# Performance work log

Measured on AMD Instinct MI355X. Metric: run time of the kernel, lower is better.

The kernel has to match this reference:

```python
import jax, jax.numpy as jnp
import numpy as np

B, N, D, H, F = 16, 512, 768, 8, 96  # D == H*F, dims preserved across layers
NEG_INF = -1e20


def setup_inputs() -> dict:
    key = jax.random.key(0)
    ks = jax.random.split(key, 16)
    embeddings = jax.random.normal(ks[0], (B, N, D), dtype=jnp.float32)
    # 0/1 float adjacency with self-loops so no row is fully masked
    adj = (jax.random.uniform(ks[1], (B, N, N)) < 0.3).astype(jnp.float32)
    adj = jnp.maximum(adj, jnp.eye(N, dtype=jnp.float32)[None])
    convo_len = jnp.full((B,), N, dtype=jnp.int32)

    def layer_params(k0, k1, k2, k3, k4, in_dim, out_dim):
        sW = (2.0 / (in_dim + out_dim)) ** 0.5  # ~xavier
        sa = (2.0 / (out_dim + 1)) ** 0.5
        sH = (2.0 / (in_dim + in_dim)) ** 0.5
        return dict(
            W=jax.random.normal(k0, (H, in_dim, out_dim)) * sW,
            b=jnp.zeros((out_dim,), jnp.float32),
            a_src=jax.random.normal(k1, (H, out_dim, 1)) * sa,
            a_dst=jax.random.normal(k2, (H, out_dim, 1)) * sa,
            Hw=jax.random.normal(k3, (in_dim, in_dim)) * sH,
            Hb=jnp.zeros((in_dim,), jnp.float32),
        )

    p0 = layer_params(ks[2], ks[3], ks[4], ks[5], ks[6], D, F)
    p1 = layer_params(ks[7], ks[8], ks[9], ks[10], ks[11], D, F)
    return {
        "embeddings": embeddings, "adj": adj, "convo_len": convo_len,
        "W0": p0["W"], "b0": p0["b"], "a_src0": p0["a_src"], "a_dst0": p0["a_dst"], "Hw0": p0["Hw"], "Hb0": p0["Hb"],
        "W1": p1["W"], "b1": p1["b"], "a_src1": p1["a_src"], "a_dst1": p1["a_dst"], "Hw1": p1["Hw"], "Hb1": p1["Hb"],
    }


def gat_layer(x, adj, W, b, a_src, a_dst, Hw, Hb):
    b_, n_, _ = x.shape
    h_, _, f_ = W.shape
    h = jnp.einsum('bni,hio->bhno', x, W)            # [B,H,N,F]
    t = jnp.tanh(h)
    s = jnp.einsum('bhno,ho->bhn', t, a_src[..., 0])  # attn_src
    d = jnp.einsum('bhno,ho->bhn', t, a_dst[..., 0])  # attn_dst
    attn = jax.nn.leaky_relu(s[:, :, :, None] + d[:, :, None, :], 0.2)  # [B,H,N,N]
    attn = jnp.where(adj[:, None, :, :] > 0, attn, NEG_INF)
    attn = jax.nn.softmax(attn, axis=-1)
    out = jnp.einsum('bhij,bhjo->bhio', attn, h) + b  # [B,H,N,F]
    # faithful to torch: transpose(0,1).contiguous().view(batch, N, -1)
    out = jnp.transpose(out, (1, 0, 2, 3)).reshape(b_, n_, h_ * f_)
    out = jax.nn.elu(out)
    gate = jax.nn.sigmoid(x @ Hw.T + Hb)
    return gate * out + (1.0 - gate) * x


def reference(embeddings, adj, convo_len,
              W0, b0, a_src0, a_dst0, Hw0, Hb0,
              W1, b1, a_src1, a_dst1, Hw1, Hb1):
    x = gat_layer(embeddings, adj, W0, b0, a_src0, a_dst0, Hw0, Hb0)
    x = gat_layer(x, adj, W1, b1, a_src1, a_dst1, Hw1, Hb1)
    return x
```

## Files before the change

kernel.cpp:

```cpp
#include <hip/hip_runtime.h>
#include <cstdint>
#include <cstddef>

typedef __attribute__((ext_vector_type(4))) float f32x4;
typedef __attribute__((ext_vector_type(8))) __bf16 bf16x8;
typedef __attribute__((ext_vector_type(8))) unsigned short u16x8;
typedef __attribute__((ext_vector_type(4))) unsigned short u16x4;

__device__ __forceinline__ unsigned short f2bf(float f){
  unsigned int u = __float_as_uint(f);
  u += 0x7fffu + ((u >> 16) & 1u);
  return (unsigned short)(u >> 16);
}
__device__ __forceinline__ float bf2f(unsigned short u){
  return __uint_as_float(((unsigned int)u) << 16);
}
__device__ __forceinline__ float fast_tanh(float x){
  const float e = __expf(2.f * x);
  return 1.f - 2.f / (e + 1.f);
}

__device__ __forceinline__ void gload_lds16(const void* g, void* l){
  __builtin_amdgcn_global_load_lds((const __attribute__((address_space(1))) void*)g,
                                   (__attribute__((address_space(3))) void*)l, 16, 0, 0);
}

__device__ __forceinline__ f32x4 mfma16(bf16x8 a, bf16x8 b, f32x4 c){
  return __builtin_amdgcn_mfma_f32_16x16x32_bf16(a, b, c, 0, 0, 0);
}

__global__ __launch_bounds__(256) void prep_kernel(const float* __restrict__ in,
                                                   unsigned short* __restrict__ out,
                                                   const float* __restrict__ adj,
                                                   unsigned int* __restrict__ mask,
                                                   const float* __restrict__ W0,
                                                   const float* __restrict__ Hw0,
                                                   unsigned short* __restrict__ Bt0,
                                                   const float* __restrict__ W1,
                                                   const float* __restrict__ Hw1,
                                                   unsigned short* __restrict__ Bt1){
  const int bid = blockIdx.x;
  if (bid < 6144){
    int i = bid * 256 + threadIdx.x;
    f32x4 v = ((const f32x4*)in)[i];
    union { unsigned short u[4]; unsigned long long ll; } o;
    #pragma unroll
    for (int e = 0; e < 4; ++e) o.u[e] = f2bf(v[e]);
    ((unsigned long long*)out)[i] = o.ll;
  } else if (bid < 6656){
    int idx = (bid - 6144) * 256 + threadIdx.x;
    const float* a = adj + (size_t)idx * 32;
    unsigned int m = 0;
    #pragma unroll
    for (int e = 0; e < 8; ++e){
      f32x4 v = *(const f32x4*)(a + e * 4);
      m |= (v[0] > 0.f ? 1u : 0u) << (e * 4);
      m |= (v[1] > 0.f ? 1u : 0u) << (e * 4 + 1);
      m |= (v[2] > 0.f ? 1u : 0u) << (e * 4 + 2);
      m |= (v[3] > 0.f ? 1u : 0u) << (e * 4 + 3);
    }
    mask[idx] = m;
  } else {
    const int rel = bid - 6656;
    const int layer = rel >= 1536;
    const int n = layer ? rel - 1536 : rel;
    const float* W  = layer ? W1  : W0;
    const float* Hw = layer ? Hw1 : Hw0;
    unsigned short* Bt = layer ? Bt1 : Bt0;
    const int k4 = threadIdx.x;
    if (k4 < 192){
      float v[4];
      if (n < 768){
        int head = n / 96, f = n % 96;
        const float* base = W + (size_t)head * 768 * 96 + f;
        #pragma unroll
        for (int e = 0; e < 4; ++e) v[e] = base[(size_t)(k4 * 4 + e) * 96];
      } else {
        f32x4 t = *(const f32x4*)(Hw + (size_t)(n - 768) * 768 + k4 * 4);
        #pragma unroll
        for (int e = 0; e < 4; ++e) v[e] = t[e];
      }
      union { unsigned short u[4]; unsigned long long ll; } o;
      #pragma unroll
      for (int e = 0; e < 4; ++e) o.u[e] = f2bf(v[e]);
      ((unsigned long long*)(Bt + (size_t)n * 768))[k4] = o.ll;
    }
  }
}

__global__ __launch_bounds__(256, 3)
void gemm_kernel(const unsigned short* __restrict__ A,
                 const unsigned short* __restrict__ Bt,
                 const float* __restrict__ Hb,
                 unsigned short* __restrict__ hT,
                 unsigned short* __restrict__ glogit){
  __shared__ __align__(16) char lds[49152];
  const int tid  = threadIdx.x;
  const int wid  = tid >> 6;
  const int lane = tid & 63;
  const int orig = blockIdx.x;
  const int wgid = (orig & 7) * 192 + (orig >> 3);
  const int mtile = wgid / 24, ntile = wgid % 24;
  const int m0 = mtile * 128, n0 = ntile * 64;
  const int wm = (wid >> 1) * 64, wn = (wid & 1) * 32;
  const int g = lane >> 4, r16 = lane & 15;

  auto stage = [&](int kt, char* base){
    #pragma unroll
    for (int c = 0; c < 4; ++c){
      const int ch = c * 256 + tid;
      const int row = ch >> 3, sp = ch & 7;
      const int cj = sp ^ (row & 7);
      gload_lds16(A + (size_t)(m0 + row) * 768 + kt * 64 + cj * 8, base + ch * 16);
    }
    #pragma unroll
    for (int c = 0; c < 2; ++c){
      const int ch = c * 256 + tid;
      const int row = ch >> 3, sp = ch & 7;
      const int cj = sp ^ (row & 7);
      gload_lds16(Bt + (size_t)(n0 + row) * 768 + kt * 64 + cj * 8, base + 16384 + ch * 16);
    }
  };

  f32x4 acc[4][2];
  #pragma unroll
  for (int i = 0; i < 4; ++i)
    #pragma unroll
    for (int j = 0; j < 2; ++j) acc[i][j] = (f32x4){0.f, 0.f, 0.f, 0.f};

  stage(0, lds);
  __syncthreads();

  for (int kt = 0; kt < 12; ++kt){
    const int cur = kt & 1;
    if (kt < 11) stage(kt + 1, lds + (cur ^ 1) * 24576);
    const char* base = lds + cur * 24576;
    bf16x8 af[4][2], bfr[2][2];
    #pragma unroll
    for (int t = 0; t < 4; ++t){
      const int rowA = wm + t * 16 + r16;
      #pragma unroll
      for (int kk = 0; kk < 2; ++kk){
        const int ckk = (kk << 2) | g;
        af[t][kk] = *(const bf16x8*)(base + rowA * 128 + ((ckk ^ (rowA & 7)) << 4));
      }
    }
    #pragma unroll
    for (int nt = 0; nt < 2; ++nt){
      const int rowB = wn + nt * 16 + r16;
      #pragma unroll
      for (int kk = 0; kk < 2; ++kk){
        const int ckk = (kk << 2) | g;
        bfr[nt][kk] = *(const bf16x8*)(base + 16384 + rowB * 128 + ((ckk ^ (rowB & 7)) << 4));
      }
    }
    #pragma unroll
    for (int mt = 0; mt < 4; ++mt)
      #pragma unroll
      for (int nt = 0; nt < 2; ++nt){
        acc[mt][nt] = mfma16(af[mt][0], bfr[nt][0], acc[mt][nt]);
        acc[mt][nt] = mfma16(af[mt][1], bfr[nt][1], acc[mt][nt]);
      }
    __syncthreads();
  }

  if (n0 < 768){
    #pragma unroll
    for (int mt = 0; mt < 4; ++mt){
      #pragma unroll
      for (int nt = 0; nt < 2; ++nt){
        const int n_local = wn + nt * 16 + r16;
        const int m_base  = wm + mt * 16 + g * 4;
        union { unsigned short u[4]; unsigned long long ll; } pk;
        #pragma unroll
        for (int r = 0; r < 4; ++r) pk.u[r] = f2bf(acc[mt][nt][r]);
        const int byte = m_base * 2;
        const int chunk = byte >> 4, o = byte & 15;
        const int pbyte = n_local * 256 + ((chunk ^ (n_local & 15)) << 4) + o;
        *(unsigned long long*)(lds + pbyte) = pk.ll;
      }
    }
    __syncthreads();
    const int b_ = m0 >> 9, nodebase = m0 & 511;
    #pragma unroll
    for (int it = 0; it < 4; ++it){
      const int ci = it * 256 + tid;
      const int row = ci >> 4, l = ci & 15;
      const int pbyte = row * 256 + (((l ^ (row & 15))) << 4);
      f32x4 v = *(const f32x4*)(lds + pbyte);
      const int n = n0 + row, head = n / 96, f = n % 96;
      *(f32x4*)(hT + (((size_t)(b_ * 8 + head)) * 96 + f) * 512 + nodebase + l * 8) = v;
    }
  } else {
    #pragma unroll
    for (int mt = 0; mt < 4; ++mt){
      #pragma unroll
      for (int nt = 0; nt < 2; ++nt){
        const int n_local = wn + nt * 16 + r16;
        const float hbv = Hb[n0 - 768 + n_local];
        const int c = n_local >> 3;
        #pragma unroll
        for (int r = 0; r < 4; ++r){
          const int m_local = wm + mt * 16 + g * 4 + r;
          const int pbyte = m_local * 128 + ((c ^ (m_local & 7)) << 4) + (n_local & 7) * 2;
          *(unsigned short*)(lds + pbyte) = f2bf(acc[mt][nt][r] + hbv);
        }
      }
    }
    __syncthreads();
    const int colbase = n0 - 768;
    #pragma unroll
    for (int it = 0; it < 4; ++it){
      const int ci = it * 256 + tid;
      const int row = ci >> 3, l = ci & 7;
      const int pbyte = row * 128 + ((l ^ (row & 7)) << 4);
      f32x4 v = *(const f32x4*)(lds + pbyte);
      *(f32x4*)(glogit + (size_t)(m0 + row) * 768 + colbase + l * 8) = v;
    }
  }
}

__global__ __launch_bounds__(256)
void sd_kernel(const unsigned short* __restrict__ hT, const float* __restrict__ asrc,
               const float* __restrict__ adst, float* __restrict__ s, float* __restrict__ d){
  const int bh = blockIdx.x;
  const int tid = threadIdx.x;
  const int head = bh & 7;
  __shared__ float as_lds[96], ad_lds[96];
  if (tid < 96) as_lds[tid] = asrc[head * 96 + tid];
  else if (tid >= 128 && tid < 224) ad_lds[tid - 128] = adst[head * 96 + tid - 128];
  __syncthreads();

  const unsigned short* hTb = hT + (size_t)bh * 96 * 512 + tid * 2;
  float s0 = 0.f, s1 = 0.f, d0 = 0.f, d1 = 0.f;
  #pragma unroll 8
  for (int f = 0; f < 96; ++f){
    const unsigned int u = *(const unsigned int*)(hTb + (size_t)f * 512);
    const float t0 = fast_tanh(bf2f((unsigned short)(u & 0xffffu)));
    const float t1 = fast_tanh(bf2f((unsigned short)(u >> 16)));
    const float a = as_lds[f], dd = ad_lds[f];
    s0 += t0 * a;  s1 += t1 * a;
    d0 += t0 * dd; d1 += t1 * dd;
  }
  const int o = (bh << 9) + tid * 2;
  *(float2*)(s + o) = make_float2(s0, s1);
  *(float2*)(d + o) = make_float2(d0, d1);
}

__global__ __launch_bounds__(256)
void attn_kernel(const float* __restrict__ s, const float* __restrict__ d,
                 const unsigned int* __restrict__ mask,
                 const unsigned short* __restrict__ hT,
                 const float* __restrict__ bias,
                 const unsigned short* __restrict__ glogit,
                 const float* __restrict__ xin,
                 float* __restrict__ outf,
                 unsigned short* __restrict__ outb,
                 int write_b){
  const int idx = blockIdx.x;
  const int bh = idx & 127, ib = idx >> 7;
  const int b  = bh >> 3;
  const int tid = threadIdx.x, wid = tid >> 6, lane = tid & 63;
  const int g = lane >> 4, r16 = lane & 15;
  const int rowbase = ib * 64 + wid * 16;

  __shared__ float d_lds[512];
  __shared__ float bias_lds[96];
  __shared__ __align__(16) char vbuf[2][12288];
  float* att_s = (float*)vbuf;

  const float* dv = d + bh * 512;
  if (tid < 128) ((f32x4*)d_lds)[tid] = ((const f32x4*)dv)[tid];
  if (tid >= 128 && tid < 152) ((f32x4*)bias_lds)[tid - 128] = ((const f32x4*)bias)[tid - 128];

  const unsigned short* hTb = hT + (size_t)bh * 96 * 512;

  auto stage = [&](int p, int bufi){
    #pragma unroll
    for (int ss2 = 0; ss2 < 3; ++ss2){
      const int ch = ss2 * 256 + tid;
      const int row = ch >> 3, slotpos = ch & 7;
      const int cj = slotpos ^ (row & 7);
      gload_lds16(hTb + (size_t)row * 512 + p * 64 + cj * 8, vbuf[bufi] + ch * 16);
    }
  };

  const int i_mine = rowbase + r16;
  const float s_i = s[bh * 512 + i_mine];

  unsigned int mw[16];
  {
    const uint4* mrow = (const uint4*)(mask + ((size_t)b * 512 + i_mine) * 16);
    uint4 a0 = mrow[0], a1 = mrow[1], a2 = mrow[2], a3 = mrow[3];
    mw[0]=a0.x; mw[1]=a0.y; mw[2]=a0.z; mw[3]=a0.w;
    mw[4]=a1.x; mw[5]=a1.y; mw[6]=a1.z; mw[7]=a1.w;
    mw[8]=a2.x; mw[9]=a2.y; mw[10]=a2.z; mw[11]=a2.w;
    mw[12]=a3.x; mw[13]=a3.y; mw[14]=a3.z; mw[15]=a3.w;
  }

  stage(0, 0);
  __syncthreads();

  float Mx = d_lds[lane];
  #pragma unroll
  for (int t = 1; t < 8; ++t) Mx = fmaxf(Mx, d_lds[t * 64 + lane]);
  #pragma unroll
  for (int o = 32; o > 0; o >>= 1) Mx = fmaxf(Mx, __shfl_xor(Mx, o));
  const float scm = s_i + Mx;
  const float m_i = fmaxf(scm, 0.2f * scm);

  f32x4 acc2[6];
  #pragma unroll
  for (int ft = 0; ft < 6; ++ft) acc2[ft] = (f32x4){0.f, 0.f, 0.f, 0.f};
  float L = 0.f;

  for (int p = 0; p < 8; ++p){
    if (p < 7) stage(p + 1, (p + 1) & 1);
    const char* vb = vbuf[p & 1];
    #pragma unroll
    for (int half = 0; half < 2; ++half){
      const int jt = p * 2 + half;
      const unsigned int w = mw[jt];
      const int j8 = jt * 32 + g * 8;
      f32x4 dA = *(const f32x4*)(d_lds + j8);
      f32x4 dB = *(const f32x4*)(d_lds + j8 + 4);
      u16x8 pa;
      #pragma unroll
      for (int e = 0; e < 4; ++e){
        float sc = s_i + dA[e]; sc = fmaxf(sc, 0.2f * sc);
        float p1 = ((w >> (g * 8 + e)) & 1u) ? __expf(sc - m_i) : 0.f;
        L += p1; pa[e] = f2bf(p1);
        float sc2 = s_i + dB[e]; sc2 = fmaxf(sc2, 0.2f * sc2);
        float p2 = ((w >> (g * 8 + 4 + e)) & 1u) ? __expf(sc2 - m_i) : 0.f;
        L += p2; pa[4 + e] = f2bf(p2);
      }
      const bf16x8 af = __builtin_bit_cast(bf16x8, pa);
      const int slot = ((half * 4 + g) ^ (r16 & 7)) * 16;
      __builtin_amdgcn_s_setprio(1);
      #pragma unroll
      for (int ft = 0; ft < 6; ++ft){
        bf16x8 vf = *(const bf16x8*)(vb + (ft * 16 + r16) * 128 + slot);
        acc2[ft] = mfma16(af, vf, acc2[ft]);
      }
      __builtin_amdgcn_s_setprio(0);
    }
    __syncthreads();
  }

  L += __shfl_xor(L, 16);
  L += __shfl_xor(L, 32);
  const float linv = 1.f / L;
  float lr[4];
  #pragma unroll
  for (int r = 0; r < 4; ++r) lr[r] = __shfl(linv, g * 4 + r);

  #pragma unroll
  for (int ft = 0; ft < 6; ++ft){
    const int f = ft * 16 + r16;
    const float bv = bias_lds[f];
    #pragma unroll
    for (int r = 0; r < 4; ++r){
      const int node = rowbase + g * 4 + r;
      att_s[((node >> 3) & 7) * 768 + (node & 7) * 96 + f] = acc2[ft][r] * lr[r] + bv;
    }
  }
  __syncthreads();

  const int hh = bh & 7;
  const int bb2 = (hh << 1) | (b >> 3);
  const int mbase = bb2 * 512 + ((b & 7) << 6) + ib * 8;
  const size_t gb4 = (size_t)mbase * 192;
  #pragma unroll
  for (int sgi = 0; sgi < 6; ++sgi){
    const int ei = sgi * 256 + tid;
    f32x4 a4 = ((const f32x4*)att_s)[ei];
    u16x4 gl = ((const u16x4*)glogit)[gb4 + ei];
    f32x4 xv = ((const f32x4*)xin)[gb4 + ei];
    f32x4 o;
    #pragma unroll
    for (int e = 0; e < 4; ++e){
      const float gate = 1.f / (1.f + __expf(-bf2f(gl[e])));
      const float a = a4[e];
      const float eluv = a > 0.f ? a : (__expf(a) - 1.f);
      o[e] = gate * eluv + (1.f - gate) * xv[e];
    }
    ((f32x4*)outf)[gb4 + ei] = o;
    if (write_b){
      union { unsigned short u[4]; unsigned long long ll; } ob;
      #pragma unroll
      for (int e = 0; e < 4; ++e) ob.u[e] = f2bf(o[e]);
      ((unsigned long long*)outb)[gb4 + ei] = ob.ll;
    }
  }
}

extern "C" void kernel_launch(void* const* d_in, const int* in_sizes, int n_in,
                              void* d_out, int out_size, void* d_ws, size_t ws_size,
                              hipStream_t stream){
  const float* emb   = (const float*)d_in[0];
  const float* adj   = (const float*)d_in[1];
  const float* W0    = (const float*)d_in[3];
  const float* b0    = (const float*)d_in[4];
  const float* asrc0 = (const float*)d_in[5];
  const float* adst0 = (const float*)d_in[6];
  const float* Hw0   = (const float*)d_in[7];
  const float* Hb0   = (const float*)d_in[8];
  const float* W1    = (const float*)d_in[9];
  const float* b1    = (const float*)d_in[10];
  const float* asrc1 = (const float*)d_in[11];
  const float* adst1 = (const float*)d_in[12];
  const float* Hw1   = (const float*)d_in[13];
  const float* Hb1   = (const float*)d_in[14];

  char* ws = (char*)d_ws;
  size_t off = 0;
  auto alloc = [&](size_t bytes){ void* p = ws + off; off += (bytes + 255) & ~(size_t)255; return p; };
  unsigned short* x0b  = (unsigned short*)alloc(8192ull * 768 * 2);
  unsigned short* Bt0  = (unsigned short*)alloc(1536ull * 768 * 2);
  unsigned short* Bt1  = (unsigned short*)alloc(1536ull * 768 * 2);
  unsigned short* hT   = (unsigned short*)alloc(8192ull * 768 * 2);
  unsigned short* glogit = (unsigned short*)alloc(8192ull * 768 * 2);
  float* sbuf          = (float*)alloc(65536ull * 4);
  float* dbuf          = (float*)alloc(65536ull * 4);
  float* x1            = (float*)alloc(8192ull * 768 * 4);
  unsigned int* mask   = (unsigned int*)alloc(16ull * 512 * 16 * 4);
  (void)ws_size; (void)in_sizes; (void)n_in; (void)out_size;

  prep_kernel<<<9728, 256, 0, stream>>>(emb, x0b, adj, mask, W0, Hw0, Bt0, W1, Hw1, Bt1);

  gemm_kernel<<<1536, 256, 0, stream>>>(x0b, Bt0, Hb0, hT, glogit);
  sd_kernel<<<128, 256, 0, stream>>>(hT, asrc0, adst0, sbuf, dbuf);
  attn_kernel<<<1024, 256, 0, stream>>>(sbuf, dbuf, mask, hT, b0, glogit, emb, x1, x0b, 1);

  gemm_kernel<<<1536, 256, 0, stream>>>(x0b, Bt1, Hb1, hT, glogit);
  sd_kernel<<<128, 256, 0, stream>>>(hT, asrc1, adst1, sbuf, dbuf);
  attn_kernel<<<1024, 256, 0, stream>>>(sbuf, dbuf, mask, hT, b1, glogit, x1, (float*)d_out, x0b, 0);
}
```

Measured before the change: 248.2 us.

## Deepen LDS prefetch pipelines with explicit vmcnt waits in GEMM and attention

The GEMM kernel now issues two stages up front and uses explicit s_waitcnt vmcnt plus raw s_barrier in place of __syncthreads. The next-next tile is loaded after compute, and the MFMA block runs at raised priority. The attention kernel moves to triple-buffered V tiles with prefetch distance two, a fully unrolled loop, the max computation moved inside the first iteration, and four split L accumulators to shorten dependency chains. The goal is to keep more global-to-LDS traffic in flight and avoid the full vmcnt(0) drains that __syncthreads forces. The risks are that the hand-written vmcnt counts depend on the exact number of loads issued per stage, and that the third buffer uses more LDS, which may lower occupancy.

```diff
diff --git a/kernel.cpp b/kernel.cpp
--- a/kernel.cpp
+++ b/kernel.cpp
@@ -28,6 +28,8 @@
 __device__ __forceinline__ f32x4 mfma16(bf16x8 a, bf16x8 b, f32x4 c){
   return __builtin_amdgcn_mfma_f32_16x16x32_bf16(a, b, c, 0, 0, 0);
 }
+
+#define SBAR()  { __builtin_amdgcn_sched_barrier(0); __builtin_amdgcn_s_barrier(); __builtin_amdgcn_sched_barrier(0); }
 
 __global__ __launch_bounds__(256) void prep_kernel(const float* __restrict__ in,
                                                    unsigned short* __restrict__ out,
@@ -129,12 +131,13 @@
     for (int j = 0; j < 2; ++j) acc[i][j] = (f32x4){0.f, 0.f, 0.f, 0.f};
 
   stage(0, lds);
-  __syncthreads();
+  stage(1, lds + 24576);
 
   for (int kt = 0; kt < 12; ++kt){
-    const int cur = kt & 1;
-    if (kt < 11) stage(kt + 1, lds + (cur ^ 1) * 24576);
-    const char* base = lds + cur * 24576;
+    if (kt < 11) { asm volatile("s_waitcnt vmcnt(6)" ::: "memory"); }
+    else         { asm volatile("s_waitcnt vmcnt(0)" ::: "memory"); }
+    SBAR();
+    const char* base = lds + (kt & 1) * 24576;
     bf16x8 af[4][2], bfr[2][2];
     #pragma unroll
     for (int t = 0; t < 4; ++t){
@@ -154,6 +157,7 @@
         bfr[nt][kk] = *(const bf16x8*)(base + 16384 + rowB * 128 + ((ckk ^ (rowB & 7)) << 4));
       }
     }
+    __builtin_amdgcn_s_setprio(1);
     #pragma unroll
     for (int mt = 0; mt < 4; ++mt)
       #pragma unroll
@@ -161,7 +165,9 @@
         acc[mt][nt] = mfma16(af[mt][0], bfr[nt][0], acc[mt][nt]);
         acc[mt][nt] = mfma16(af[mt][1], bfr[nt][1], acc[mt][nt]);
       }
-    __syncthreads();
+    __builtin_amdgcn_s_setprio(0);
+    SBAR();
+    if (kt < 10) stage(kt + 2, lds + (kt & 1) * 24576);
   }
 
   if (n0 < 768){
@@ -266,7 +272,7 @@
 
   __shared__ float d_lds[512];
   __shared__ float bias_lds[96];
-  __shared__ __align__(16) char vbuf[2][12288];
+  __shared__ __align__(16) char vbuf[3][12288];
   float* att_s = (float*)vbuf;
 
   const float* dv = d + bh * 512;
@@ -299,24 +305,31 @@
   }
 
   stage(0, 0);
-  __syncthreads();
-
-  float Mx = d_lds[lane];
-  #pragma unroll
-  for (int t = 1; t < 8; ++t) Mx = fmaxf(Mx, d_lds[t * 64 + lane]);
-  #pragma unroll
-  for (int o = 32; o > 0; o >>= 1) Mx = fmaxf(Mx, __shfl_xor(Mx, o));
-  const float scm = s_i + Mx;
-  const float m_i = fmaxf(scm, 0.2f * scm);
-
+  stage(1, 1);
+  asm volatile("s_waitcnt lgkmcnt(0)" ::: "memory");
+
+  float m_i;
   f32x4 acc2[6];
   #pragma unroll
   for (int ft = 0; ft < 6; ++ft) acc2[ft] = (f32x4){0.f, 0.f, 0.f, 0.f};
-  float L = 0.f;
-
+  float L0 = 0.f, L1 = 0.f, L2 = 0.f, L3 = 0.f;
+
+  #pragma unroll
   for (int p = 0; p < 8; ++p){
-    if (p < 7) stage(p + 1, (p + 1) & 1);
-    const char* vb = vbuf[p & 1];
+    if (p < 7) { asm volatile("s_waitcnt vmcnt(3)" ::: "memory"); }
+    else       { asm volatile("s_waitcnt vmcnt(0)" ::: "memory"); }
+    SBAR();
+    if (p == 0){
+      float Mx = d_lds[lane];
+      #pragma unroll
+      for (int t = 1; t < 8; ++t) Mx = fmaxf(Mx, d_lds[t * 64 + lane]);
+      #pragma unroll
+      for (int o = 32; o > 0; o >>= 1) Mx = fmaxf(Mx, __shfl_xor(Mx, o));
+      const float scm = s_i + Mx;
+      m_i = fmaxf(scm, 0.2f * scm);
+    }
+    if (p < 6) stage(p + 2, (p + 2) % 3);
+    const char* vb = vbuf[p % 3];
     #pragma unroll
     for (int half = 0; half < 2; ++half){
       const int jt = p * 2 + half;
@@ -329,10 +342,12 @@
       for (int e = 0; e < 4; ++e){
         float sc = s_i + dA[e]; sc = fmaxf(sc, 0.2f * sc);
         float p1 = ((w >> (g * 8 + e)) & 1u) ? __expf(sc - m_i) : 0.f;
-        L += p1; pa[e] = f2bf(p1);
         float sc2 = s_i + dB[e]; sc2 = fmaxf(sc2, 0.2f * sc2);
         float p2 = ((w >> (g * 8 + 4 + e)) & 1u) ? __expf(sc2 - m_i) : 0.f;
-        L += p2; pa[4 + e] = f2bf(p2);
+        if (e == 0){ L0 += p1; L0 += p2; } else if (e == 1){ L1 += p1; L1 += p2; }
+        else if (e == 2){ L2 += p1; L2 += p2; } else { L3 += p1; L3 += p2; }
+        pa[e] = f2bf(p1);
+        pa[4 + e] = f2bf(p2);
       }
       const bf16x8 af = __builtin_bit_cast(bf16x8, pa);
       const int slot = ((half * 4 + g) ^ (r16 & 7)) * 16;
@@ -344,9 +359,10 @@
       }
       __builtin_amdgcn_s_setprio(0);
     }
-    __syncthreads();
-  }
-
+  }
+  __syncthreads();
+
+  float L = (L0 + L1) + (L2 + L3);
   L += __shfl_xor(L, 16);
   L += __shfl_xor(L, 32);
   const float linv = 1.f / L;
```

Result: no change. 246.7 us (-0.6%).
